# Kernel optimization log

Measured on AMD Instinct MI355X. Metric: run time of the kernel, lower is better.

## Reference

```python
import math
import jax, jax.numpy as jnp
import numpy as np

EMBED_DIM = 512
NUM_HEADS = 8
HEAD_DIM = EMBED_DIM // NUM_HEADS
NUM_EDGE_TYPES = 10
N = 2048  # nodes
B = 1


def setup_inputs() -> dict:
    key = jax.random.key(0)
    ks = jax.random.split(key, 8)
    s = 1.0 / math.sqrt(EMBED_DIM)
    return {
        "query": jax.random.normal(ks[0], (N, B, EMBED_DIM), jnp.float32),
        "key": jax.random.normal(ks[1], (N, B, EMBED_DIM), jnp.float32),
        "value": jax.random.normal(ks[2], (N, B, EMBED_DIM), jnp.float32),
        "edge_id_mat": jax.random.randint(ks[3], (N, N), 0, NUM_EDGE_TYPES, jnp.int32),
        "in_proj_weight": jax.random.normal(ks[4], (3 * EMBED_DIM, EMBED_DIM), jnp.float32) * s,
        "in_proj_bias": jnp.zeros((3 * EMBED_DIM,), jnp.float32),
        "out_proj_weight": jax.random.normal(ks[5], (EMBED_DIM, EMBED_DIM), jnp.float32) * s,
        "out_proj_bias": jnp.zeros((EMBED_DIM,), jnp.float32),
        "edge_embs_K": jax.random.normal(ks[6], (NUM_EDGE_TYPES, HEAD_DIM), jnp.float32),
    }


def reference(query, key, value, edge_id_mat, in_proj_weight, in_proj_bias,
              out_proj_weight, out_proj_bias, edge_embs_K):
    L, Bsz, E = query.shape
    H, hd = NUM_HEADS, HEAD_DIM
    w_q, w_k, w_v = jnp.split(in_proj_weight, 3, axis=0)
    b_q, b_k, b_v = jnp.split(in_proj_bias, 3)
    q = query @ w_q.T + b_q   # (L, B, E)
    k = key @ w_k.T + b_k
    v = value @ w_v.T + b_v

    def split_heads(x):
        # (L, B, E) -> (B*H, L, hd)  (matches torch view(L, B*H, hd).transpose(0,1))
        return x.reshape(L, Bsz * H, hd).transpose(1, 0, 2)

    q = split_heads(q) / math.sqrt(hd)  # torch scales by sqrt(E=head_dim)
    k = split_heads(k)
    v = split_heads(v)

    attn = jnp.einsum('bnd,bmd->bnm', q, k)  # (B*H, L, L)

    # edge-type score bias: edge_attn[b,i,j] = q[b,i,:] . edge_embs_K[edge_id_mat[i,j], :]
    # computed efficiently as per-type scores then a gather (avoids (L,L,hd) tensor)
    type_scores = jnp.einsum('bnd,td->bnt', q, edge_embs_K)  # (B*H, L, T)
    idx = jnp.broadcast_to(edge_id_mat[None, :, :], attn.shape)
    edge_attn = jnp.take_along_axis(type_scores, idx, axis=2)  # (B*H, L, L)
    attn = jax.nn.softmax(attn + edge_attn, axis=-1)

    out = jnp.einsum('bnm,bmd->bnd', attn, v)           # (B*H, L, hd)
    out = out.transpose(1, 0, 2).reshape(L, Bsz, E)      # (L, B, E)
    out = out @ out_proj_weight.T + out_proj_bias
    return out
```

## Files before the change

kernel.cpp:

```cpp
#include <hip/hip_runtime.h>
#include <hip/hip_bf16.h>

#define NHEAD 8
#define SEQ   2048
#define HD    64
#define EMB   512
#define NTYPE 10
#define JSPLIT 4

typedef unsigned short u16;
typedef __attribute__((ext_vector_type(8))) short short8;
typedef __attribute__((ext_vector_type(4))) float float4v;

union F8 { short8 v; uint4 u4; u16 us[8]; };

__device__ __forceinline__ float bf2f(u16 u){
  union { unsigned u; float f; } w; w.u = ((unsigned)u) << 16; return w.f;
}
__device__ __forceinline__ u16 f2bf(float f){
  union { float f; unsigned u; } w; w.f = f;
  unsigned u = w.u;
  u += 0x7fffu + ((u >> 16) & 1u);
  return (u16)(u >> 16);
}
__device__ __forceinline__ unsigned pk2(float a, float b){
  return (unsigned)f2bf(a) | ((unsigned)f2bf(b) << 16);
}

__device__ __forceinline__ void gload_lds16(const u16* g, u16* l){
  __builtin_amdgcn_global_load_lds(
      (const __attribute__((address_space(1))) unsigned int*)g,
      (__attribute__((address_space(3))) unsigned int*)l, 16, 0, 0);
}

__global__ __launch_bounds__(256) void cvt_kernel(
    const float* __restrict__ q, const float* __restrict__ k, const float* __restrict__ v,
    const float* __restrict__ ipw, const float* __restrict__ opw,
    u16* __restrict__ Abf, u16* __restrict__ Wbf, u16* __restrict__ OWbf)
{
  const int gid = blockIdx.x * 256 + threadIdx.x;
  const int e8 = gid * 8;
  const float* src; u16* dst; int off;
  if      (e8 < 1048576) { src = q;   dst = Abf;            off = e8; }
  else if (e8 < 2097152) { src = k;   dst = Abf + 1048576;  off = e8 - 1048576; }
  else if (e8 < 3145728) { src = v;   dst = Abf + 2097152;  off = e8 - 2097152; }
  else if (e8 < 3932160) { src = ipw; dst = Wbf;            off = e8 - 3145728; }
  else                   { src = opw; dst = OWbf;           off = e8 - 3932160; }
  float4 a = *(const float4*)(src + off);
  float4 b = *(const float4*)(src + off + 4);
  uint4 p; p.x = pk2(a.x, a.y); p.y = pk2(a.z, a.w);
           p.z = pk2(b.x, b.y); p.w = pk2(b.z, b.w);
  *(uint4*)(dst + off) = p;
}

__global__ __launch_bounds__(256) void pack_eid_kernel(const int* __restrict__ eid,
                                                       unsigned* __restrict__ out){
  int i = blockIdx.x * 256 + threadIdx.x;
  int4 v = ((const int4*)eid)[i];
  out[i] = (unsigned)(v.x & 0xff) | ((unsigned)(v.y & 0xff) << 8) |
           ((unsigned)(v.z & 0xff) << 16) | ((unsigned)(v.w & 0xff) << 24);
}

template<int WNF, int MODE>
__global__ __launch_bounds__(256) void gemm_bt(
    const u16* __restrict__ Aall, const u16* __restrict__ Bw,
    const float* __restrict__ bias,
    u16* __restrict__ Qs, u16* __restrict__ Kb, u16* __restrict__ Vb,
    float* __restrict__ outF)
{
  constexpr int BN = WNF * 32;
  constexpr int K  = 512;
  __shared__ u16 lds[128 * 32 + BN * 32];
  u16* As = lds;
  u16* Bs = lds + 128 * 32;

  const int t = threadIdx.x, w = t >> 6, lane = t & 63, lr = lane & 15, lg = lane >> 4;
  const int n0 = blockIdx.x * BN;
  const int m0 = blockIdx.y * 128;
  const int wm = w >> 1, wn = w & 1;

  int z = 0;
  const u16* A = Aall;
  if (MODE == 0) { z = n0 >> 9; A = Aall + (size_t)z * (2048 * 512); }

  float4v acc[4][WNF];
#pragma unroll
  for (int mi = 0; mi < 4; mi++)
#pragma unroll
    for (int ni = 0; ni < WNF; ni++) acc[mi][ni] = (float4v){0.f, 0.f, 0.f, 0.f};

  const int rb = lane >> 2, kb = (lane & 3) * 8;

  for (int k0 = 0; k0 < K; k0 += 32) {
    __syncthreads();
#pragma unroll
    for (int c = 0; c < 2; c++) {
      const int ci = w * 2 + c;
      gload_lds16(A + (size_t)(m0 + ci * 16 + rb) * K + k0 + kb, As + ci * 512);
    }
#pragma unroll
    for (int c = 0; c < WNF / 2; c++) {
      const int ci = w * (WNF / 2) + c;
      gload_lds16(Bw + (size_t)(n0 + ci * 16 + rb) * K + k0 + kb, Bs + ci * 512);
    }
    __syncthreads();

    F8 af[4], bfr[WNF];
#pragma unroll
    for (int mi = 0; mi < 4; mi++)
      af[mi].u4 = *(const uint4*)(As + (wm * 64 + mi * 16 + lr) * 32 + lg * 8);
#pragma unroll
    for (int ni = 0; ni < WNF; ni++)
      bfr[ni].u4 = *(const uint4*)(Bs + (wn * (BN / 2) + ni * 16 + lr) * 32 + lg * 8);
#pragma unroll
    for (int mi = 0; mi < 4; mi++)
#pragma unroll
      for (int ni = 0; ni < WNF; ni++)
        acc[mi][ni] = __builtin_amdgcn_mfma_f32_16x16x32_bf16(af[mi].v, bfr[ni].v, acc[mi][ni], 0, 0, 0);
  }

  if (MODE == 0) {
    u16* O = (z == 0) ? Qs : ((z == 1) ? Kb : Vb);
    const float scale = (z == 0) ? 0.125f : 1.0f;
#pragma unroll
    for (int mi = 0; mi < 4; mi++) {
#pragma unroll
      for (int ni = 0; ni < WNF; ni++) {
        const int n = n0 + wn * (BN / 2) + ni * 16 + lr;
        const int e = n & 511, h = e >> 6, d = e & 63;
        const float bb = bias[n];
        const int mb = m0 + wm * 64 + mi * 16 + lg * 4;
        if (z < 2) {
#pragma unroll
          for (int r = 0; r < 4; r++)
            O[((size_t)h * SEQ + mb + r) * HD + d] = f2bf((acc[mi][ni][r] + bb) * scale);
        } else {
          ushort4 pk;
          pk.x = f2bf(acc[mi][ni][0] + bb); pk.y = f2bf(acc[mi][ni][1] + bb);
          pk.z = f2bf(acc[mi][ni][2] + bb); pk.w = f2bf(acc[mi][ni][3] + bb);
          *(ushort4*)(O + ((size_t)(h * HD + d)) * SEQ + mb) = pk;
        }
      }
    }
  } else {
#pragma unroll
    for (int mi = 0; mi < 4; mi++) {
#pragma unroll
      for (int ni = 0; ni < WNF; ni++) {
        const int n = n0 + wn * (BN / 2) + ni * 16 + lr;
        const float bb = bias[n];
        const int mb = m0 + wm * 64 + mi * 16 + lg * 4;
#pragma unroll
        for (int r = 0; r < 4; r++)
          outF[(size_t)(mb + r) * EMB + n] = acc[mi][ni][r] + bb;
      }
    }
  }
}

__global__ __launch_bounds__(256) void attn_kernel(
    const u16* __restrict__ Qs, const u16* __restrict__ Kb, const u16* __restrict__ Vb,
    const unsigned char* __restrict__ eidp, const float* __restrict__ EK,
    float* __restrict__ Upart, float* __restrict__ mpart, float* __restrict__ lpart)
{
  __shared__ u16 Kt[64][72];
  __shared__ u16 Vt[64][72];
  __shared__ u16 Pl[4][16][72];
  __shared__ unsigned char eidt[64][64];
  __shared__ float tsl[64][12];
  __shared__ float ekl[NTYPE][64];
  __shared__ float mrow[64], lrow[64], frow[64];

  const int t = threadIdx.x;
  const int wave = t >> 6, lane = t & 63, lr = lane & 15, lg = lane >> 4;
  const int i0 = blockIdx.x * 64;
  const int h  = blockIdx.y;
  const int z  = blockIdx.z;

  for (int i = t; i < NTYPE * 64; i += 256) ekl[i >> 6][i & 63] = EK[i];
  if (t < 64) { mrow[t] = -1e30f; lrow[t] = 0.f; }
  __syncthreads();

  {
    const int row = t >> 2, tt = t & 3;
    const u16* qr = Qs + ((size_t)h * SEQ + i0 + row) * HD;
    float a0 = 0.f, a1 = 0.f, a2 = 0.f;
    for (int d0 = 0; d0 < HD; d0 += 8) {
      uint4 qq = *(const uint4*)(qr + d0);
      const u16* qu = (const u16*)&qq;
#pragma unroll
      for (int e = 0; e < 8; e++) {
        float qf = bf2f(qu[e]);
        a0 += qf * ekl[tt][d0 + e];
        a1 += qf * ekl[tt + 4][d0 + e];
        a2 += qf * ekl[(tt < 2) ? (tt + 8) : 8][d0 + e];
      }
    }
    tsl[row][tt] = a0; tsl[row][tt + 4] = a1;
    if (tt < 2) tsl[row][tt + 8] = a2;
  }

  F8 qf[2];
#pragma unroll
  for (int kc = 0; kc < 2; kc++)
    qf[kc].u4 = *(const uint4*)(Qs + ((size_t)h * SEQ + i0 + wave * 16 + lr) * HD + kc * 32 + lg * 8);

  float4v ao[4];
#pragma unroll
  for (int d = 0; d < 4; d++) ao[d] = (float4v){0.f, 0.f, 0.f, 0.f};

  const int jbase = z * (SEQ / JSPLIT);
  for (int jt = 0; jt < (SEQ / JSPLIT) / 64; jt++) {
    const int j0 = jbase + jt * 64;
    __syncthreads();
    {
      const int row = t >> 2, dc = (t & 3) * 16;
      const u16* kp = Kb + ((size_t)h * SEQ + j0 + row) * HD + dc;
      *(uint4*)&Kt[row][dc]     = *(const uint4*)kp;
      *(uint4*)&Kt[row][dc + 8] = *(const uint4*)(kp + 8);
      const u16* vp = Vb + ((size_t)(h * HD + row)) * SEQ + j0 + dc;
      *(uint4*)&Vt[row][dc]     = *(const uint4*)vp;
      *(uint4*)&Vt[row][dc + 8] = *(const uint4*)(vp + 8);
      *(uint4*)&eidt[row][dc] = *(const uint4*)(eidp + (size_t)(i0 + row) * SEQ + j0 + dc);
    }
    __syncthreads();

    float4v sacc[4];
#pragma unroll
    for (int c = 0; c < 4; c++) sacc[c] = (float4v){0.f, 0.f, 0.f, 0.f};
#pragma unroll
    for (int kc = 0; kc < 2; kc++) {
#pragma unroll
      for (int c = 0; c < 4; c++) {
        F8 kf; kf.u4 = *(const uint4*)&Kt[c * 16 + lr][kc * 32 + lg * 8];
        sacc[c] = __builtin_amdgcn_mfma_f32_16x16x32_bf16(qf[kc].v, kf.v, sacc[c], 0, 0, 0);
      }
    }

    float pv_[4][4];
    float rmax[4] = {-1e30f, -1e30f, -1e30f, -1e30f};
#pragma unroll
    for (int c = 0; c < 4; c++) {
#pragma unroll
      for (int r = 0; r < 4; r++) {
        const int row = wave * 16 + lg * 4 + r;
        float s = sacc[c][r] + tsl[row][eidt[row][c * 16 + lr]];
        pv_[c][r] = s;
        rmax[r] = fmaxf(rmax[r], s);
      }
    }
#pragma unroll
    for (int mm = 1; mm < 16; mm <<= 1) {
#pragma unroll
      for (int r = 0; r < 4; r++) rmax[r] = fmaxf(rmax[r], __shfl_xor(rmax[r], mm));
    }
    float mnew[4], fct[4], rsum[4] = {0.f, 0.f, 0.f, 0.f};
#pragma unroll
    for (int r = 0; r < 4; r++) {
      const int row = wave * 16 + lg * 4 + r;
      const float mo = mrow[row];
      mnew[r] = fmaxf(mo, rmax[r]);
      fct[r] = __expf(mo - mnew[r]);
    }
#pragma unroll
    for (int c = 0; c < 4; c++) {
#pragma unroll
      for (int r = 0; r < 4; r++) {
        float p = __expf(pv_[c][r] - mnew[r]);
        pv_[c][r] = p;
        rsum[r] += p;
      }
    }
#pragma unroll
    for (int mm = 1; mm < 16; mm <<= 1) {
#pragma unroll
      for (int r = 0; r < 4; r++) rsum[r] += __shfl_xor(rsum[r], mm);
    }
    if (lr == 0) {
#pragma unroll
      for (int r = 0; r < 4; r++) {
        const int row = wave * 16 + lg * 4 + r;
        mrow[row] = mnew[r];
        lrow[row] = lrow[row] * fct[r] + rsum[r];
        frow[row] = fct[r];
      }
    }
#pragma unroll
    for (int c = 0; c < 4; c++) {
#pragma unroll
      for (int r = 0; r < 4; r++)
        Pl[wave][lg * 4 + r][c * 16 + lr] = f2bf(pv_[c][r]);
    }
    const float fo = frow[wave * 16 + lr];
#pragma unroll
    for (int d = 0; d < 4; d++) {
#pragma unroll
      for (int r = 0; r < 4; r++) ao[d][r] *= fo;
    }
#pragma unroll
    for (int kc = 0; kc < 2; kc++) {
      F8 pf; pf.u4 = *(const uint4*)&Pl[wave][lr][kc * 32 + lg * 8];
#pragma unroll
      for (int db = 0; db < 4; db++) {
        F8 vf; vf.u4 = *(const uint4*)&Vt[db * 16 + lr][kc * 32 + lg * 8];
        ao[db] = __builtin_amdgcn_mfma_f32_16x16x32_bf16(vf.v, pf.v, ao[db], 0, 0, 0);
      }
    }
  }

  {
    const size_t base = (((size_t)z * NHEAD + h) * SEQ + i0) * HD;
#pragma unroll
    for (int db = 0; db < 4; db++) {
#pragma unroll
      for (int r = 0; r < 4; r++) {
        const int d = db * 16 + lg * 4 + r;
        const int n = wave * 16 + lr;
        Upart[base + (size_t)n * HD + d] = ao[db][r];
      }
    }
    __syncthreads();
    if (t < 64) {
      mpart[((size_t)z * NHEAD + h) * SEQ + i0 + t] = mrow[t];
      lpart[((size_t)z * NHEAD + h) * SEQ + i0 + t] = lrow[t];
    }
  }
}

__global__ __launch_bounds__(256) void combine_kernel(
    const float* __restrict__ Upart, const float* __restrict__ mpart,
    const float* __restrict__ lpart, u16* __restrict__ AObf)
{
  const int rid = blockIdx.x * 4 + (threadIdx.x >> 6);
  const int d = threadIdx.x & 63;
  float mm[JSPLIT];
  float M = -1e30f;
#pragma unroll
  for (int zz = 0; zz < JSPLIT; zz++) {
    mm[zz] = mpart[(size_t)zz * NHEAD * SEQ + rid];
    M = fmaxf(M, mm[zz]);
  }
  float Ls = 0.f, U = 0.f;
#pragma unroll
  for (int zz = 0; zz < JSPLIT; zz++) {
    const float w = __expf(mm[zz] - M);
    Ls += w * lpart[(size_t)zz * NHEAD * SEQ + rid];
    U  += w * Upart[((size_t)zz * NHEAD * SEQ + rid) * HD + d];
  }
  const int hh = rid >> 11;
  const int n = rid & (SEQ - 1);
  AObf[(size_t)n * EMB + hh * HD + d] = f2bf(U / Ls);
}

extern "C" void kernel_launch(void* const* d_in, const int* in_sizes, int n_in,
                              void* d_out, int out_size, void* d_ws, size_t ws_size,
                              hipStream_t stream)
{
  const float* query = (const float*)d_in[0];
  const float* key_  = (const float*)d_in[1];
  const float* value = (const float*)d_in[2];
  const int*   eid   = (const int*)d_in[3];
  const float* ipw   = (const float*)d_in[4];
  const float* ipb   = (const float*)d_in[5];
  const float* opw   = (const float*)d_in[6];
  const float* opb   = (const float*)d_in[7];
  const float* ek    = (const float*)d_in[8];
  float* out = (float*)d_out;

  char* ws = (char*)d_ws;
  u16* Abf  = (u16*)ws;            ws += (size_t)3 * SEQ * EMB * 2;
  u16* Wbf  = (u16*)ws;            ws += (size_t)3 * EMB * EMB * 2;
  u16* OWbf = (u16*)ws;            ws += (size_t)EMB * EMB * 2;
  u16* Qs = (u16*)ws;              ws += (size_t)NHEAD * SEQ * HD * 2;
  u16* Kb = (u16*)ws;              ws += (size_t)NHEAD * SEQ * HD * 2;
  u16* Vb = (u16*)ws;              ws += (size_t)NHEAD * SEQ * HD * 2;
  unsigned char* eidp = (unsigned char*)ws; ws += (size_t)SEQ * SEQ;
  float* Upart = (float*)ws;       ws += (size_t)JSPLIT * NHEAD * SEQ * HD * 4;
  float* mpart = (float*)ws;       ws += (size_t)JSPLIT * NHEAD * SEQ * 4;
  float* lpart = (float*)ws;       ws += (size_t)JSPLIT * NHEAD * SEQ * 4;
  u16* AObf    = (u16*)ws;         ws += (size_t)SEQ * EMB * 2;

  cvt_kernel<<<dim3(2048), dim3(256), 0, stream>>>(query, key_, value, ipw, opw, Abf, Wbf, OWbf);
  pack_eid_kernel<<<dim3(SEQ * SEQ / 4 / 256), dim3(256), 0, stream>>>(eid, (unsigned*)eidp);
  gemm_bt<4, 0><<<dim3(3 * EMB / 128, SEQ / 128), dim3(256), 0, stream>>>(
      Abf, Wbf, ipb, Qs, Kb, Vb, nullptr);
  attn_kernel<<<dim3(SEQ / 64, NHEAD, JSPLIT), dim3(256), 0, stream>>>(
      Qs, Kb, Vb, eidp, ek, Upart, mpart, lpart);
  combine_kernel<<<dim3(NHEAD * SEQ / 4), dim3(256), 0, stream>>>(Upart, mpart, lpart, AObf);
  gemm_bt<2, 1><<<dim3(EMB / 64, SEQ / 128), dim3(256), 0, stream>>>(
      AObf, OWbf, opb, nullptr, nullptr, nullptr, out);
}
```

Baseline: 168.7 us.

## Prefetch next K/V/edge tile into registers, swizzle edge LDS, halve split, fuse prep

The attention loop now loads the next K, V and edge-id tile into registers while computing the current one, and writes them to LDS after a barrier. This replaces the load-then-sync pattern and is meant to hide global latency. The edge-id LDS tile is XOR-swizzled, and the type-score table is padded, both to cut bank conflicts. JSPLIT drops from 4 to 2, which halves the partial-output traffic but also halves the attention grid. The conversion and edge-packing kernels are merged into one launch.

Result: faster. 162.3 us (-3.8%).

```diff
diff --git a/kernel.cpp b/kernel.cpp
--- a/kernel.cpp
+++ b/kernel.cpp
@@ -6,7 +6,7 @@
 #define HD    64
 #define EMB   512
 #define NTYPE 10
-#define JSPLIT 4
+#define JSPLIT 2
 
 typedef unsigned short u16;
 typedef __attribute__((ext_vector_type(8))) short short8;
@@ -33,32 +33,33 @@
       (__attribute__((address_space(3))) unsigned int*)l, 16, 0, 0);
 }
 
-__global__ __launch_bounds__(256) void cvt_kernel(
+__global__ __launch_bounds__(256) void prep_kernel(
     const float* __restrict__ q, const float* __restrict__ k, const float* __restrict__ v,
     const float* __restrict__ ipw, const float* __restrict__ opw,
-    u16* __restrict__ Abf, u16* __restrict__ Wbf, u16* __restrict__ OWbf)
+    const int* __restrict__ eid,
+    u16* __restrict__ Abf, u16* __restrict__ Wbf, u16* __restrict__ OWbf,
+    unsigned* __restrict__ eidp)
 {
   const int gid = blockIdx.x * 256 + threadIdx.x;
-  const int e8 = gid * 8;
-  const float* src; u16* dst; int off;
-  if      (e8 < 1048576) { src = q;   dst = Abf;            off = e8; }
-  else if (e8 < 2097152) { src = k;   dst = Abf + 1048576;  off = e8 - 1048576; }
-  else if (e8 < 3145728) { src = v;   dst = Abf + 2097152;  off = e8 - 2097152; }
-  else if (e8 < 3932160) { src = ipw; dst = Wbf;            off = e8 - 3145728; }
-  else                   { src = opw; dst = OWbf;           off = e8 - 3932160; }
-  float4 a = *(const float4*)(src + off);
-  float4 b = *(const float4*)(src + off + 4);
-  uint4 p; p.x = pk2(a.x, a.y); p.y = pk2(a.z, a.w);
-           p.z = pk2(b.x, b.y); p.w = pk2(b.z, b.w);
-  *(uint4*)(dst + off) = p;
-}
-
-__global__ __launch_bounds__(256) void pack_eid_kernel(const int* __restrict__ eid,
-                                                       unsigned* __restrict__ out){
-  int i = blockIdx.x * 256 + threadIdx.x;
-  int4 v = ((const int4*)eid)[i];
-  out[i] = (unsigned)(v.x & 0xff) | ((unsigned)(v.y & 0xff) << 8) |
-           ((unsigned)(v.z & 0xff) << 16) | ((unsigned)(v.w & 0xff) << 24);
+  if (blockIdx.x < 2048) {
+    const int e8 = gid * 8;
+    const float* src; u16* dst; int off;
+    if      (e8 < 1048576) { src = q;   dst = Abf;            off = e8; }
+    else if (e8 < 2097152) { src = k;   dst = Abf + 1048576;  off = e8 - 1048576; }
+    else if (e8 < 3145728) { src = v;   dst = Abf + 2097152;  off = e8 - 2097152; }
+    else if (e8 < 3932160) { src = ipw; dst = Wbf;            off = e8 - 3145728; }
+    else                   { src = opw; dst = OWbf;           off = e8 - 3932160; }
+    float4 a = *(const float4*)(src + off);
+    float4 b = *(const float4*)(src + off + 4);
+    uint4 p; p.x = pk2(a.x, a.y); p.y = pk2(a.z, a.w);
+             p.z = pk2(b.x, b.y); p.w = pk2(b.z, b.w);
+    *(uint4*)(dst + off) = p;
+  } else {
+    const int i = gid - 524288;
+    int4 vv = ((const int4*)eid)[i];
+    eidp[i] = (unsigned)(vv.x & 0xff) | ((unsigned)(vv.y & 0xff) << 8) |
+              ((unsigned)(vv.z & 0xff) << 16) | ((unsigned)(vv.w & 0xff) << 24);
+  }
 }
 
 template<int WNF, int MODE>
@@ -167,7 +168,7 @@
   __shared__ u16 Vt[64][72];
   __shared__ u16 Pl[4][16][72];
   __shared__ unsigned char eidt[64][64];
-  __shared__ float tsl[64][12];
+  __shared__ float tsl[64][13];
   __shared__ float ekl[NTYPE][64];
   __shared__ float mrow[64], lrow[64], frow[64];
 
@@ -209,21 +210,34 @@
 #pragma unroll
   for (int d = 0; d < 4; d++) ao[d] = (float4v){0.f, 0.f, 0.f, 0.f};
 
+  const int srow = t >> 2, sdc = (t & 3) * 16;
+  const int sec = sdc ^ (((t >> 4) & 3) << 4);
   const int jbase = z * (SEQ / JSPLIT);
-  for (int jt = 0; jt < (SEQ / JSPLIT) / 64; jt++) {
-    const int j0 = jbase + jt * 64;
+  const int NT = (SEQ / JSPLIT) / 64;
+
+  uint4 kp0, kp1, vp0, vp1, ep0;
+  {
+    const u16* kp = Kb + ((size_t)h * SEQ + jbase + srow) * HD + sdc;
+    kp0 = *(const uint4*)kp; kp1 = *(const uint4*)(kp + 8);
+    const u16* vp = Vb + ((size_t)(h * HD + srow)) * SEQ + jbase + sdc;
+    vp0 = *(const uint4*)vp; vp1 = *(const uint4*)(vp + 8);
+    ep0 = *(const uint4*)(eidp + (size_t)(i0 + srow) * SEQ + jbase + sdc);
+    *(uint4*)&Kt[srow][sdc] = kp0; *(uint4*)&Kt[srow][sdc + 8] = kp1;
+    *(uint4*)&Vt[srow][sdc] = vp0; *(uint4*)&Vt[srow][sdc + 8] = vp1;
+    *(uint4*)&eidt[srow][sec] = ep0;
+  }
+
+  for (int jt = 0; jt < NT; jt++) {
     __syncthreads();
-    {
-      const int row = t >> 2, dc = (t & 3) * 16;
-      const u16* kp = Kb + ((size_t)h * SEQ + j0 + row) * HD + dc;
-      *(uint4*)&Kt[row][dc]     = *(const uint4*)kp;
-      *(uint4*)&Kt[row][dc + 8] = *(const uint4*)(kp + 8);
-      const u16* vp = Vb + ((size_t)(h * HD + row)) * SEQ + j0 + dc;
-      *(uint4*)&Vt[row][dc]     = *(const uint4*)vp;
-      *(uint4*)&Vt[row][dc + 8] = *(const uint4*)(vp + 8);
-      *(uint4*)&eidt[row][dc] = *(const uint4*)(eidp + (size_t)(i0 + row) * SEQ + j0 + dc);
-    }
-    __syncthreads();
+
+    if (jt + 1 < NT) {
+      const int jn = jbase + (jt + 1) * 64;
+      const u16* kp = Kb + ((size_t)h * SEQ + jn + srow) * HD + sdc;
+      kp0 = *(const uint4*)kp; kp1 = *(const uint4*)(kp + 8);
+      const u16* vp = Vb + ((size_t)(h * HD + srow)) * SEQ + jn + sdc;
+      vp0 = *(const uint4*)vp; vp1 = *(const uint4*)(vp + 8);
+      ep0 = *(const uint4*)(eidp + (size_t)(i0 + srow) * SEQ + jn + sdc);
+    }
 
     float4v sacc[4];
 #pragma unroll
@@ -241,10 +255,11 @@
     float rmax[4] = {-1e30f, -1e30f, -1e30f, -1e30f};
 #pragma unroll
     for (int c = 0; c < 4; c++) {
+      const int ec = ((c ^ lg) << 4) + lr;
 #pragma unroll
       for (int r = 0; r < 4; r++) {
         const int row = wave * 16 + lg * 4 + r;
-        float s = sacc[c][r] + tsl[row][eidt[row][c * 16 + lr]];
+        float s = sacc[c][r] + tsl[row][eidt[row][ec]];
         pv_[c][r] = s;
         rmax[r] = fmaxf(rmax[r], s);
       }
@@ -305,6 +320,13 @@
         F8 vf; vf.u4 = *(const uint4*)&Vt[db * 16 + lr][kc * 32 + lg * 8];
         ao[db] = __builtin_amdgcn_mfma_f32_16x16x32_bf16(vf.v, pf.v, ao[db], 0, 0, 0);
       }
+    }
+
+    __syncthreads();
+    if (jt + 1 < NT) {
+      *(uint4*)&Kt[srow][sdc] = kp0; *(uint4*)&Kt[srow][sdc + 8] = kp1;
+      *(uint4*)&Vt[srow][sdc] = vp0; *(uint4*)&Vt[srow][sdc + 8] = vp1;
+      *(uint4*)&eidt[srow][sec] = ep0;
     }
   }
 
@@ -380,8 +402,8 @@
   float* lpart = (float*)ws;       ws += (size_t)JSPLIT * NHEAD * SEQ * 4;
   u16* AObf    = (u16*)ws;         ws += (size_t)SEQ * EMB * 2;
 
-  cvt_kernel<<<dim3(2048), dim3(256), 0, stream>>>(query, key_, value, ipw, opw, Abf, Wbf, OWbf);
-  pack_eid_kernel<<<dim3(SEQ * SEQ / 4 / 256), dim3(256), 0, stream>>>(eid, (unsigned*)eidp);
+  prep_kernel<<<dim3(6144), dim3(256), 0, stream>>>(
+      query, key_, value, ipw, opw, eid, Abf, Wbf, OWbf, (unsigned*)eidp);
   gemm_bt<4, 0><<<dim3(3 * EMB / 128, SEQ / 128), dim3(256), 0, stream>>>(
       Abf, Wbf, ipb, Qs, Kb, Vb, nullptr);
   attn_kernel<<<dim3(SEQ / 64, NHEAD, JSPLIT), dim3(256), 0, stream>>>(
```
